# Kernel tuning notes

Hardware: AMD Instinct MI355X
Metric: run time of the kernel (lower is better)

## Reference

```python
import jax, jax.numpy as jnp
import numpy as np

N = 50000      # nodes
E = 600000     # edges (before self-loops)
F_IN = 128     # num_node_features
HID = 64       # hidden_channels
HEADS = 4      # num_heads
ACT = 32       # action_dim
SENT = 768     # sentence embedding dim (fc1 input)


def setup_inputs() -> dict:
    key = jax.random.key(0)
    ks = jax.random.split(key, 32)
    rn = lambda k, s, sc=0.05: jax.random.normal(k, s, jnp.float32) * sc
    return {
        "x": jax.random.normal(ks[0], (N, F_IN), jnp.float32),
        "edge_index": jax.random.randint(ks[1], (2, E), 0, N, dtype=jnp.int32),
        "sentence_emb": jax.random.normal(ks[2], (1, SENT), jnp.float32),
        "active_node_idx": 123,
        "step": 3,
        # conv1: GATConv(F_IN -> HID, heads=HEADS, concat=True)
        "W1": rn(ks[3], (F_IN, HEADS * HID)),
        "att_src1": rn(ks[4], (HEADS, HID)),
        "att_dst1": rn(ks[5], (HEADS, HID)),
        "b1": jnp.zeros((HEADS * HID,), jnp.float32),
        # conv2: GATConv(HEADS*HID -> HID, heads=1, concat=False)
        "W2": rn(ks[6], (HEADS * HID, HID)),
        "att_src2": rn(ks[7], (1, HID)),
        "att_dst2": rn(ks[8], (1, HID)),
        "b2": jnp.zeros((HID,), jnp.float32),
        "fc0_w": rn(ks[9], (1, HID)), "fc0_b": jnp.zeros((HID,), jnp.float32),
        "fc1_w": rn(ks[10], (SENT, HID)), "fc1_b": jnp.zeros((HID,), jnp.float32),
        "fc2_w": rn(ks[11], (HID, HID)), "fc2_b": jnp.zeros((HID,), jnp.float32),
        "fc3_w": rn(ks[12], (2 * HID, HID)), "fc3_b": jnp.zeros((HID,), jnp.float32),
        "val_w": rn(ks[13], (HID, 1)), "val_b": jnp.zeros((1,), jnp.float32),
        "adv_w": rn(ks[14], (HID, ACT)), "adv_b": jnp.zeros((ACT,), jnp.float32),
        "ln_h_g": jnp.ones((HID,), jnp.float32), "ln_h_b": jnp.zeros((HID,), jnp.float32),
        "ln_f_g": jnp.ones((2 * HID,), jnp.float32), "ln_f_b": jnp.zeros((2 * HID,), jnp.float32),
        "ln_a_g": jnp.ones((HEADS * HID,), jnp.float32), "ln_a_b": jnp.zeros((HEADS * HID,), jnp.float32),
    }


def layernorm(x, g, b, eps=1e-5):
    mu = jnp.mean(x, axis=-1, keepdims=True)
    var = jnp.mean((x - mu) ** 2, axis=-1, keepdims=True)
    return (x - mu) / jnp.sqrt(var + eps) * g + b


def gat_layer(h_in, src, dst, W, a_src, a_dst, bias, concat):
    """PyG GATConv (eval mode): gather -> edge score -> segment softmax -> scatter-add."""
    n = h_in.shape[0]
    heads, ch = a_src.shape
    h = (h_in @ W).reshape(n, heads, ch)                      # [N,H,C]
    es = jnp.einsum('nhc,hc->nh', h, a_src)                   # alpha_src per node
    ed = jnp.einsum('nhc,hc->nh', h, a_dst)                   # alpha_dst per node
    e = jax.nn.leaky_relu(es[src] + ed[dst], 0.2)             # [Etot,H]
    m = jax.ops.segment_max(e, dst, num_segments=n)           # stable softmax per dst
    ex = jnp.exp(e - m[dst])
    denom = jax.ops.segment_sum(ex, dst, num_segments=n) + 1e-16
    alpha = ex / denom[dst]                                   # [Etot,H]
    out = jax.ops.segment_sum(h[src] * alpha[:, :, None], dst, num_segments=n)
    out = out.reshape(n, heads * ch) if concat else out.mean(axis=1)
    return out + bias, alpha


def reference(x, edge_index, sentence_emb, active_node_idx, step,
              W1, att_src1, att_dst1, b1, W2, att_src2, att_dst2, b2,
              fc0_w, fc0_b, fc1_w, fc1_b, fc2_w, fc2_b, fc3_w, fc3_b,
              val_w, val_b, adv_w, adv_b,
              ln_h_g, ln_h_b, ln_f_g, ln_f_b, ln_a_g, ln_a_b):
    n = x.shape[0]
    loops = jnp.arange(n, dtype=edge_index.dtype)             # PyG add_self_loops=True
    src = jnp.concatenate([edge_index[0], loops])
    dst = jnp.concatenate([edge_index[1], loops])

    # step embedding: fc0((step+1)*0.01) -> relu -> LN
    steps = jnp.full((1, 1), (step + 1) * 0.01, jnp.float32)
    steps = layernorm(jax.nn.relu(steps @ fc0_w + fc0_b), ln_h_g, ln_h_b)

    # sentence embedding path (F.normalize result is discarded in the original)
    sent = layernorm(jax.nn.relu(sentence_emb @ fc1_w + fc1_b), ln_h_g, ln_h_b)
    sent = sent + steps
    sent = layernorm(jax.nn.relu(sent @ fc2_w + fc2_b), ln_h_g, ln_h_b)

    # two GAT layers
    h1, _ = gat_layer(x, src, dst, W1, att_src1, att_dst1, b1, concat=True)
    h1 = layernorm(jax.nn.elu(h1), ln_a_g, ln_a_b)
    h2, alpha = gat_layer(h1, src, dst, W2, att_src2, att_dst2, b2, concat=False)
    h2 = layernorm(h2, ln_h_g, ln_h_b)

    # dueling head on active node
    anf = jnp.concatenate([h2[active_node_idx][None, :], sent], axis=1)   # [1, 2*HID]
    anf = layernorm(anf, ln_f_g, ln_f_b)
    anf = layernorm(jax.nn.relu(anf @ fc3_w + fc3_b), ln_h_g, ln_h_b)
    val = anf @ val_w + val_b
    adv = anf @ adv_w + adv_b
    logits = jnp.tanh(val + adv - adv.mean())
    return logits, h2, alpha
```

## Files before the change

kernel.cpp:

```cpp
#include <hip/hip_runtime.h>
#include <cstdint>
#include <cstddef>

#define DEV __device__ __forceinline__

static constexpr int NN  = 50000;
static constexpr int EE  = 600000;
static constexpr int ET  = 650000;
static constexpr int CAP = 96;

typedef __attribute__((ext_vector_type(8))) short bf16x8;
typedef __attribute__((ext_vector_type(4))) float f32x4;
typedef __attribute__((ext_vector_type(4))) int   i32x4;

DEV float wsum(float v){
  #pragma unroll
  for (int o = 32; o > 0; o >>= 1) v += __shfl_xor(v, o, 64);
  return v;
}
DEV float wmaxr(float v){
  #pragma unroll
  for (int o = 32; o > 0; o >>= 1) v = fmaxf(v, __shfl_xor(v, o, 64));
  return v;
}
DEV float lrelu(float x){ return x > 0.f ? x : 0.2f * x; }
DEV float eluf(float x){ return x > 0.f ? x : expm1f(x); }
DEV float ln64(float v, const float* g, const float* b, int lane){
  float mu  = wsum(v) * (1.f/64.f);
  float d   = v - mu;
  float var = wsum(d*d) * (1.f/64.f);
  return d * rsqrtf(var + 1e-5f) * g[lane] + b[lane];
}
DEV unsigned int bf16u(float f){
  unsigned int u = __float_as_uint(f);
  return (u + 0x7fffu + ((u >> 16) & 1u)) >> 16;
}
DEV float bfl(unsigned int lo16){ return __uint_as_float(lo16 << 16); }

__global__ void bucket_fill(const int* __restrict__ ei,
                            int* __restrict__ cnt,
                            int* __restrict__ bucket){
  int e = blockIdx.x * blockDim.x + threadIdx.x;
  if (e >= ET) return;
  int src, dst;
  if (e < EE){ src = ei[e]; dst = ei[EE + e]; } else { src = dst = e - EE; }
  int pos = atomicAdd(&cnt[dst], 1);
  if (pos < CAP) bucket[(size_t)dst * CAP + pos] = src;
}

__global__ __launch_bounds__(256) void pack_both(const float* __restrict__ W1,
                                                 const float* __restrict__ W2,
                                                 short* __restrict__ Wp1,
                                                 short* __restrict__ Wp2){
  int tid = blockIdx.x * 256 + threadIdx.x;
  if (tid < 4096){
    int lane = tid & 63, ks = (tid >> 6) & 3, mb = tid >> 8;
    int col  = mb * 16 + (lane & 15);
    int krow = ks * 32 + (lane >> 4) * 8;
    #pragma unroll
    for (int j = 0; j < 8; j++)
      Wp1[(size_t)tid * 8 + j] = (short)bf16u(W1[(size_t)(krow + j) * 256 + col]);
  } else if (tid < 4096 + 2048){
    int t2 = tid - 4096;
    int lane = t2 & 63, ks = (t2 >> 6) & 7, mb = t2 >> 9;
    int col  = mb * 16 + (lane & 15);
    int krow = ks * 32 + (lane >> 4) * 8;
    #pragma unroll
    for (int j = 0; j < 8; j++)
      Wp2[(size_t)t2 * 8 + j] = (short)bf16u(W2[(size_t)(krow + j) * 64 + col]);
  }
}

template<int KSTEPS, int MBLKS, int NH, bool INF32>
__global__ __launch_bounds__(256) void mfma_gemm_att(const short* __restrict__ Wp,
                                                     const float* __restrict__ Xf,
                                                     const unsigned short* __restrict__ Xh,
                                                     unsigned short* __restrict__ Cb,
                                                     const float* __restrict__ asrc,
                                                     const float* __restrict__ adst,
                                                     float* __restrict__ es,
                                                     float* __restrict__ ed, int M){
  constexpr int K = KSTEPS * 32, N = MBLKS * 16;
  int lane  = threadIdx.x & 63;
  int wv    = threadIdx.x >> 6;
  int quad  = lane >> 4;
  int node  = blockIdx.x * 64 + wv * 16 + (lane & 15);
  bool nv   = node < M;
  int nodec = nv ? node : M - 1;

  f32x4 acc[MBLKS];
  #pragma unroll
  for (int m = 0; m < MBLKS; m++) acc[m] = (f32x4){0.f, 0.f, 0.f, 0.f};

  #pragma unroll
  for (int ks = 0; ks < KSTEPS; ks++){
    int k0 = ks * 32 + quad * 8;
    bf16x8 bfrag;
    if (INF32){
      float4 u = *(const float4*)(Xf + (size_t)nodec * K + k0);
      float4 v = *(const float4*)(Xf + (size_t)nodec * K + k0 + 4);
      i32x4 bi;
      bi.x = (int)(bf16u(u.x) | (bf16u(u.y) << 16));
      bi.y = (int)(bf16u(u.z) | (bf16u(u.w) << 16));
      bi.z = (int)(bf16u(v.x) | (bf16u(v.y) << 16));
      bi.w = (int)(bf16u(v.z) | (bf16u(v.w) << 16));
      bfrag = __builtin_bit_cast(bf16x8, bi);
    } else {
      bfrag = *(const bf16x8*)(Xh + (size_t)nodec * K + k0);
    }
    #pragma unroll
    for (int mb = 0; mb < MBLKS; mb++){
      bf16x8 afrag = *(const bf16x8*)(Wp + ((size_t)(mb * KSTEPS + ks) * 64 + lane) * 8);
      acc[mb] = __builtin_amdgcn_mfma_f32_16x16x32_bf16(afrag, bfrag, acc[mb], 0, 0, 0);
    }
  }

  if (nv){
    unsigned short* crow = Cb + (size_t)node * N;
    #pragma unroll
    for (int mb = 0; mb < MBLKS; mb++){
      uint2 p;
      p.x = bf16u(acc[mb][0]) | (bf16u(acc[mb][1]) << 16);
      p.y = bf16u(acc[mb][2]) | (bf16u(acc[mb][3]) << 16);
      *(uint2*)(crow + mb * 16 + quad * 4) = p;
    }
  }

  float ps[NH], pd[NH];
  #pragma unroll
  for (int h = 0; h < NH; h++){ ps[h] = 0.f; pd[h] = 0.f; }
  #pragma unroll
  for (int mb = 0; mb < MBLKS; mb++){
    int h = (NH == 1) ? 0 : (mb >> 2);
    #pragma unroll
    for (int r = 0; r < 4; r++){
      int c = mb * 16 + quad * 4 + r;
      ps[h] = fmaf(acc[mb][r], asrc[c], ps[h]);
      pd[h] = fmaf(acc[mb][r], adst[c], pd[h]);
    }
  }
  #pragma unroll
  for (int h = 0; h < NH; h++){
    ps[h] += __shfl_xor(ps[h], 16, 64); ps[h] += __shfl_xor(ps[h], 32, 64);
    pd[h] += __shfl_xor(pd[h], 16, 64); pd[h] += __shfl_xor(pd[h], 32, 64);
  }
  if (quad == 0 && nv){
    if (NH == 4){
      *(float4*)(es + (size_t)node * 4) = make_float4(ps[0], ps[1], ps[2], ps[3]);
      *(float4*)(ed + (size_t)node * 4) = make_float4(pd[0], pd[1], pd[2], pd[3]);
    } else {
      es[node] = ps[0];
      ed[node] = pd[0];
    }
  }
}

DEV void acc4u(uint2 g, float q, float& ax, float& ay, float& az, float& aw){
  ax = fmaf(__uint_as_float(g.x << 16),         q, ax);
  ay = fmaf(__uint_as_float(g.x & 0xffff0000u), q, ay);
  az = fmaf(__uint_as_float(g.y << 16),         q, az);
  aw = fmaf(__uint_as_float(g.y & 0xffff0000u), q, aw);
}

__global__ __launch_bounds__(256) void agg1_kernel(const int* __restrict__ cnt,
                                                   const int* __restrict__ bucket,
                                                   const unsigned short* __restrict__ H1b,
                                                   const float* __restrict__ es,
                                                   const float* __restrict__ ed,
                                                   const float* __restrict__ b1,
                                                   const float* __restrict__ lng,
                                                   const float* __restrict__ lnb,
                                                   unsigned short* __restrict__ h1b, int n){
  __shared__ float wsh4[4][64][4];
  __shared__ int   ssh[4][64];
  int wv   = threadIdx.x >> 6;
  int wid  = (blockIdx.x * blockDim.x + threadIdx.x) >> 6;
  int lane = threadIdx.x & 63;
  if (wid >= n) return;
  int deg = min(cnt[wid], CAP);
  const int* base = bucket + (size_t)wid * CAP;
  const float4 edv = *(const float4*)(ed + (size_t)wid * 4);

  float v0, v1, v2, v3;

  if (deg <= 64){
    bool vld = lane < deg;
    int srcl = vld ? base[lane] : 0;
    float4 e4 = vld ? *(const float4*)(es + (size_t)srcl * 4)
                    : make_float4(-1e30f, -1e30f, -1e30f, -1e30f);
    float e0 = vld ? lrelu(e4.x + edv.x) : -1e30f;
    float e1 = vld ? lrelu(e4.y + edv.y) : -1e30f;
    float e2 = vld ? lrelu(e4.z + edv.z) : -1e30f;
    float e3 = vld ? lrelu(e4.w + edv.w) : -1e30f;
    float m0 = wmaxr(e0), m1 = wmaxr(e1), m2 = wmaxr(e2), m3 = wmaxr(e3);
    float w0 = vld ? __expf(e0 - m0) : 0.f;
    float w1 = vld ? __expf(e1 - m1) : 0.f;
    float w2 = vld ? __expf(e2 - m2) : 0.f;
    float w3 = vld ? __expf(e3 - m3) : 0.f;
    w0 /= (wsum(w0) + 1e-16f);
    w1 /= (wsum(w1) + 1e-16f);
    w2 /= (wsum(w2) + 1e-16f);
    w3 /= (wsum(w3) + 1e-16f);
    ssh[wv][lane] = srcl;
    *(float4*)&wsh4[wv][lane][0] = make_float4(w0, w1, w2, w3);
    __builtin_amdgcn_wave_barrier();

    int h = lane >> 4;
    int lane4 = lane * 4;
    float ax = 0.f, ay = 0.f, az = 0.f, aw = 0.f;
    int t = 0;
    for (; t + 4 <= deg; t += 4){
      int a0 = ssh[wv][t],     a1 = ssh[wv][t + 1];
      int a2 = ssh[wv][t + 2], a3 = ssh[wv][t + 3];
      float q0 = wsh4[wv][t][h],     q1 = wsh4[wv][t + 1][h];
      float q2 = wsh4[wv][t + 2][h], q3 = wsh4[wv][t + 3][h];
      uint2 g0 = *(const uint2*)(H1b + (size_t)a0 * 256 + lane4);
      uint2 g1 = *(const uint2*)(H1b + (size_t)a1 * 256 + lane4);
      uint2 g2 = *(const uint2*)(H1b + (size_t)a2 * 256 + lane4);
      uint2 g3 = *(const uint2*)(H1b + (size_t)a3 * 256 + lane4);
      acc4u(g0, q0, ax, ay, az, aw);
      acc4u(g1, q1, ax, ay, az, aw);
      acc4u(g2, q2, ax, ay, az, aw);
      acc4u(g3, q3, ax, ay, az, aw);
    }
    for (; t < deg; t++){
      int a0 = ssh[wv][t];
      float q0 = wsh4[wv][t][h];
      uint2 g0 = *(const uint2*)(H1b + (size_t)a0 * 256 + lane4);
      acc4u(g0, q0, ax, ay, az, aw);
    }
    float4 bb = *(const float4*)(b1 + lane4);
    v0 = eluf(ax + bb.x); v1 = eluf(ay + bb.y);
    v2 = eluf(az + bb.z); v3 = eluf(aw + bb.w);
    float mu = wsum(v0 + v1 + v2 + v3) * (1.f/256.f);
    float q  = (v0-mu)*(v0-mu) + (v1-mu)*(v1-mu) + (v2-mu)*(v2-mu) + (v3-mu)*(v3-mu);
    float rstd = rsqrtf(wsum(q) * (1.f/256.f) + 1e-5f);
    float4 g4v = *(const float4*)(lng + lane4);
    float4 bo  = *(const float4*)(lnb + lane4);
    uint2 p;
    p.x = bf16u((v0-mu)*rstd*g4v.x + bo.x) | (bf16u((v1-mu)*rstd*g4v.y + bo.y) << 16);
    p.y = bf16u((v2-mu)*rstd*g4v.z + bo.z) | (bf16u((v3-mu)*rstd*g4v.w + bo.w) << 16);
    *(uint2*)(h1b + (size_t)wid * 256 + lane4) = p;
    return;
  }

  float m0 = -1e30f, m1 = -1e30f, m2 = -1e30f, m3 = -1e30f;
  for (int j = lane; j < deg; j += 64){
    int src = base[j];
    float4 e4 = *(const float4*)(es + (size_t)src * 4);
    m0 = fmaxf(m0, lrelu(e4.x + edv.x));
    m1 = fmaxf(m1, lrelu(e4.y + edv.y));
    m2 = fmaxf(m2, lrelu(e4.z + edv.z));
    m3 = fmaxf(m3, lrelu(e4.w + edv.w));
  }
  m0 = wmaxr(m0); m1 = wmaxr(m1); m2 = wmaxr(m2); m3 = wmaxr(m3);
  float acc0 = 0.f, acc1 = 0.f, acc2 = 0.f, acc3 = 0.f;
  float den0 = 0.f, den1 = 0.f, den2 = 0.f, den3 = 0.f;
  for (int j = 0; j < deg; j++){
    int src = base[j];
    float4 e4 = *(const float4*)(es + (size_t)src * 4);
    float x0 = __expf(lrelu(e4.x + edv.x) - m0);
    float x1 = __expf(lrelu(e4.y + edv.y) - m1);
    float x2 = __expf(lrelu(e4.z + edv.z) - m2);
    float x3 = __expf(lrelu(e4.w + edv.w) - m3);
    den0 += x0; den1 += x1; den2 += x2; den3 += x3;
    const unsigned short* hp = H1b + (size_t)src * 256;
    acc0 = fmaf(bfl(hp[lane]),       x0, acc0);
    acc1 = fmaf(bfl(hp[64 + lane]),  x1, acc1);
    acc2 = fmaf(bfl(hp[128 + lane]), x2, acc2);
    acc3 = fmaf(bfl(hp[192 + lane]), x3, acc3);
  }
  v0 = eluf(acc0 / (den0 + 1e-16f) + b1[lane]);
  v1 = eluf(acc1 / (den1 + 1e-16f) + b1[64 + lane]);
  v2 = eluf(acc2 / (den2 + 1e-16f) + b1[128 + lane]);
  v3 = eluf(acc3 / (den3 + 1e-16f) + b1[192 + lane]);
  float mu = wsum(v0 + v1 + v2 + v3) * (1.f/256.f);
  float q  = (v0-mu)*(v0-mu) + (v1-mu)*(v1-mu) + (v2-mu)*(v2-mu) + (v3-mu)*(v3-mu);
  float rstd = rsqrtf(wsum(q) * (1.f/256.f) + 1e-5f);
  unsigned short* o = h1b + (size_t)wid * 256;
  o[lane]       = (unsigned short)bf16u((v0-mu)*rstd*lng[lane]       + lnb[lane]);
  o[64 + lane]  = (unsigned short)bf16u((v1-mu)*rstd*lng[64 + lane]  + lnb[64 + lane]);
  o[128 + lane] = (unsigned short)bf16u((v2-mu)*rstd*lng[128 + lane] + lnb[128 + lane]);
  o[192 + lane] = (unsigned short)bf16u((v3-mu)*rstd*lng[192 + lane] + lnb[192 + lane]);
}

DEV float agg2_slow(const int* base, int deg, float edv,
                    const unsigned short* H2b, const float* es,
                    int lane, float& m_out, float& den_out){
  float m = -1e30f;
  for (int j = lane; j < deg; j += 64)
    m = fmaxf(m, lrelu(es[base[j]] + edv));
  m = wmaxr(m);
  float den = 0.f;
  for (int j = lane; j < deg; j += 64)
    den += __expf(lrelu(es[base[j]] + edv) - m);
  den = wsum(den) + 1e-16f;
  float acc = 0.f;
  for (int j = 0; j < deg; j++){
    int src = base[j];
    float a = __expf(lrelu(es[src] + edv) - m) / den;
    acc = fmaf(bfl(H2b[(size_t)src * 64 + lane]), a, acc);
  }
  m_out = m; den_out = den;
  return acc;
}

__global__ __launch_bounds__(256) void agg2_head(const int* __restrict__ cnt,
                                                 const int* __restrict__ bucket,
                                                 const unsigned short* __restrict__ H2b,
                                                 const float* __restrict__ es,
                                                 const float* __restrict__ ed,
                                                 const float* __restrict__ b2,
                                                 const float* __restrict__ lng,
                                                 const float* __restrict__ lnb,
                                                 const float* __restrict__ semb,
                                                 const int* __restrict__ active,
                                                 const int* __restrict__ stepp,
                                                 const float* __restrict__ fc0w, const float* __restrict__ fc0b,
                                                 const float* __restrict__ fc1w, const float* __restrict__ fc1b,
                                                 const float* __restrict__ fc2w, const float* __restrict__ fc2b,
                                                 const float* __restrict__ fc3w, const float* __restrict__ fc3b,
                                                 const float* __restrict__ valw, const float* __restrict__ valb,
                                                 const float* __restrict__ advw, const float* __restrict__ advb,
                                                 const float* __restrict__ lnhg, const float* __restrict__ lnhb,
                                                 const float* __restrict__ lnfg, const float* __restrict__ lnfb,
                                                 float* __restrict__ h2out,
                                                 float2* __restrict__ mden,
                                                 float* __restrict__ logits, int n){
  __shared__ float shh[192];
  int wpair = (blockIdx.x * blockDim.x + threadIdx.x) >> 6;
  int lane  = threadIdx.x & 63;
  int n0 = wpair * 2, n1 = wpair * 2 + 1;
  if (n0 >= n) return;
  bool has1 = n1 < n;

  int deg0 = min(cnt[n0], CAP);
  int deg1 = has1 ? min(cnt[n1], CAP) : 0;
  const int* base0 = bucket + (size_t)n0 * CAP;
  const int* base1 = bucket + (size_t)n1 * CAP;
  float edv0 = ed[n0];
  float edv1 = has1 ? ed[n1] : 0.f;
  float acc0 = 0.f, acc1 = 0.f;

  if (deg0 <= 64 && deg1 <= 64){
    bool v0 = lane < deg0;
    int s0 = v0 ? base0[lane] : 0;
    float e0 = v0 ? lrelu(es[s0] + edv0) : -1e30f;
    float m0 = wmaxr(e0);
    float w0 = v0 ? __expf(e0 - m0) : 0.f;
    float den0 = wsum(w0) + 1e-16f;
    float wl0 = v0 ? w0 / den0 : 0.f;
    bool v1 = lane < deg1;
    int s1 = v1 ? base1[lane] : 0;
    float e1 = v1 ? lrelu(es[s1] + edv1) : -1e30f;
    float m1 = wmaxr(e1);
    float w1 = v1 ? __expf(e1 - m1) : 0.f;
    float den1 = wsum(w1) + 1e-16f;
    float wl1 = v1 ? w1 / den1 : 0.f;
    if (lane == 0){
      mden[n0] = make_float2(m0, den0);
      if (has1) mden[n1] = make_float2(m1, den1);
    }

    int dmax = max(deg0, deg1);
    int t = 0;
    for (; t + 2 <= dmax; t += 2){
      int a00 = __shfl(s0, t, 64),   a01 = __shfl(s0, t + 1, 64);
      int a10 = __shfl(s1, t, 64),   a11 = __shfl(s1, t + 1, 64);
      float q00 = __shfl(wl0, t, 64), q01 = __shfl(wl0, t + 1, 64);
      float q10 = __shfl(wl1, t, 64), q11 = __shfl(wl1, t + 1, 64);
      float h00 = bfl(H2b[(size_t)a00 * 64 + lane]);
      float h01 = bfl(H2b[(size_t)a01 * 64 + lane]);
      float h10 = bfl(H2b[(size_t)a10 * 64 + lane]);
      float h11 = bfl(H2b[(size_t)a11 * 64 + lane]);
      acc0 = fmaf(h00, q00, acc0); acc0 = fmaf(h01, q01, acc0);
      acc1 = fmaf(h10, q10, acc1); acc1 = fmaf(h11, q11, acc1);
    }
    for (; t < dmax; t++){
      int a00 = __shfl(s0, t, 64);
      int a10 = __shfl(s1, t, 64);
      float q00 = __shfl(wl0, t, 64);
      float q10 = __shfl(wl1, t, 64);
      acc0 = fmaf(bfl(H2b[(size_t)a00 * 64 + lane]), q00, acc0);
      acc1 = fmaf(bfl(H2b[(size_t)a10 * 64 + lane]), q10, acc1);
    }
  } else {
    float m0, den0, m1 = 0.f, den1 = 1.f;
    acc0 = agg2_slow(base0, deg0, edv0, H2b, es, lane, m0, den0);
    if (has1) acc1 = agg2_slow(base1, deg1, edv1, H2b, es, lane, m1, den1);
    if (lane == 0){
      mden[n0] = make_float2(m0, den0);
      if (has1) mden[n1] = make_float2(m1, den1);
    }
  }

  float va = acc0 + b2[lane];
  float mua = wsum(va) * (1.f/64.f);
  float da = va - mua;
  float rsa = rsqrtf(wsum(da*da) * (1.f/64.f) + 1e-5f);
  float h2v0 = da * rsa * lng[lane] + lnb[lane];
  h2out[(size_t)n0 * 64 + lane] = h2v0;
  float h2v1 = 0.f;
  if (has1){
    float vb = acc1 + b2[lane];
    float mub = wsum(vb) * (1.f/64.f);
    float db = vb - mub;
    float rsb = rsqrtf(wsum(db*db) * (1.f/64.f) + 1e-5f);
    h2v1 = db * rsb * lng[lane] + lnb[lane];
    h2out[(size_t)n1 * 64 + lane] = h2v1;
  }

  int actv = active[0];
  if (n0 == actv || n1 == actv){
    int t = lane;
    float h2v = (n0 == actv) ? h2v0 : h2v1;

    float sval = (float)(stepp[0] + 1) * 0.01f;
    float stepsv = ln64(fmaxf(fmaf(sval, fc0w[t], fc0b[t]), 0.f), lnhg, lnhb, t);

    float acc1h = fc1b[t];
    #pragma unroll 8
    for (int k = 0; k < 768; k++) acc1h = fmaf(semb[k], fc1w[k * 64 + t], acc1h);
    float sentv = ln64(fmaxf(acc1h, 0.f), lnhg, lnhb, t) + stepsv;
    shh[t] = sentv;
    __builtin_amdgcn_wave_barrier();
    float acc2h = fc2b[t];
    #pragma unroll 8
    for (int k = 0; k < 64; k++) acc2h = fmaf(shh[k], fc2w[k * 64 + t], acc2h);
    __builtin_amdgcn_wave_barrier();
    float sent2 = ln64(fmaxf(acc2h, 0.f), lnhg, lnhb, t);

    float c0 = h2v, c1 = sent2;
    float mu2 = wsum(c0 + c1) * (1.f/128.f);
    float q2  = (c0-mu2)*(c0-mu2) + (c1-mu2)*(c1-mu2);
    float rs2 = rsqrtf(wsum(q2) * (1.f/128.f) + 1e-5f);
    shh[t]      = (c0-mu2)*rs2*lnfg[t]      + lnfb[t];
    shh[64 + t] = (c1-mu2)*rs2*lnfg[64 + t] + lnfb[64 + t];
    __builtin_amdgcn_wave_barrier();

    float acc3h = fc3b[t];
    #pragma unroll 8
    for (int k = 0; k < 128; k++) acc3h = fmaf(shh[k], fc3w[k * 64 + t], acc3h);
    float a2v = ln64(fmaxf(acc3h, 0.f), lnhg, lnhb, t);
    shh[128 + t] = a2v;
    __builtin_amdgcn_wave_barrier();

    float val = wsum(a2v * valw[t]) + valb[0];
    float advv = 0.f;
    if (t < 32){
      advv = advb[t];
      #pragma unroll 8
      for (int k = 0; k < 64; k++) advv = fmaf(shh[128 + k], advw[k * 32 + t], advv);
    }
    float am = wsum(t < 32 ? advv : 0.f) * (1.f/32.f);
    if (t < 32) logits[t] = tanhf(val + advv - am);
  }
}

__global__ __launch_bounds__(256) void edge_alpha(const int* __restrict__ ei,
                                                  const float* __restrict__ es,
                                                  const float* __restrict__ ed,
                                                  const float2* __restrict__ mden,
                                                  float* __restrict__ alpha_out){
  int e = blockIdx.x * blockDim.x + threadIdx.x;
  if (e >= ET) return;
  int src, dst;
  if (e < EE){ src = ei[e]; dst = ei[EE + e]; } else { src = dst = e - EE; }
  float2 md = mden[dst];
  float sc = lrelu(es[src] + ed[dst]);
  alpha_out[e] = __expf(sc - md.x) / md.y;
}

extern "C" void kernel_launch(void* const* d_in, const int* in_sizes, int n_in,
                              void* d_out, int out_size, void* d_ws, size_t ws_size,
                              hipStream_t stream) {
  const float* x     = (const float*)d_in[0];
  const int*   ei    = (const int*)  d_in[1];
  const float* semb  = (const float*)d_in[2];
  const int*   act   = (const int*)  d_in[3];
  const int*   step  = (const int*)  d_in[4];
  const float* W1    = (const float*)d_in[5];
  const float* as1   = (const float*)d_in[6];
  const float* ad1   = (const float*)d_in[7];
  const float* b1    = (const float*)d_in[8];
  const float* W2    = (const float*)d_in[9];
  const float* as2   = (const float*)d_in[10];
  const float* ad2   = (const float*)d_in[11];
  const float* b2    = (const float*)d_in[12];
  const float* fc0w  = (const float*)d_in[13];
  const float* fc0b  = (const float*)d_in[14];
  const float* fc1w  = (const float*)d_in[15];
  const float* fc1b  = (const float*)d_in[16];
  const float* fc2w  = (const float*)d_in[17];
  const float* fc2b  = (const float*)d_in[18];
  const float* fc3w  = (const float*)d_in[19];
  const float* fc3b  = (const float*)d_in[20];
  const float* valw  = (const float*)d_in[21];
  const float* valb  = (const float*)d_in[22];
  const float* advw  = (const float*)d_in[23];
  const float* advb  = (const float*)d_in[24];
  const float* lnhg  = (const float*)d_in[25];
  const float* lnhb  = (const float*)d_in[26];
  const float* lnfg  = (const float*)d_in[27];
  const float* lnfb  = (const float*)d_in[28];
  const float* lnag  = (const float*)d_in[29];
  const float* lnab  = (const float*)d_in[30];

  char* ws = (char*)d_ws;
  size_t o = 0;
  auto alloc = [&](size_t bytes) -> void* {
    o = (o + 255) & ~(size_t)255;
    void* p = ws + o;
    o += bytes;
    return p;
  };
  int*   cnt     = (int*)  alloc((size_t)NN * 4);
  int*   bucket  = (int*)  alloc((size_t)NN * CAP * 4);
  short* Wp1     = (short*)alloc((size_t)4096 * 8 * 2);
  short* Wp2     = (short*)alloc((size_t)2048 * 8 * 2);
  unsigned short* H1b = (unsigned short*)alloc((size_t)NN * 256 * 2);
  unsigned short* h1b = (unsigned short*)alloc((size_t)NN * 256 * 2);
  float* es1     = (float*)alloc((size_t)NN * 16);
  float* ed1     = (float*)alloc((size_t)NN * 16);
  float2* mden   = (float2*)alloc((size_t)NN * 8);
  unsigned short* H2b = H1b;
  float* es2 = es1;
  float* ed2 = ed1;

  float* logits    = (float*)d_out;
  float* h2out     = (float*)d_out + 32;
  float* alpha_out = (float*)d_out + 32 + (size_t)NN * 64;

  hipMemsetAsync(cnt, 0, (size_t)NN * 4, stream);
  bucket_fill<<<(ET + 255) / 256, 256, 0, stream>>>(ei, cnt, bucket);
  pack_both<<<24, 256, 0, stream>>>(W1, W2, Wp1, Wp2);

  mfma_gemm_att<4, 16, 4, true><<<(NN + 63) / 64, 256, 0, stream>>>(
      Wp1, x, nullptr, H1b, as1, ad1, es1, ed1, NN);
  agg1_kernel<<<NN / 4, 256, 0, stream>>>(cnt, bucket, H1b, es1, ed1, b1, lnag, lnab, h1b, NN);

  mfma_gemm_att<8, 4, 1, false><<<(NN + 63) / 64, 256, 0, stream>>>(
      Wp2, nullptr, h1b, H2b, as2, ad2, es2, ed2, NN);
  agg2_head<<<(NN + 7) / 8, 256, 0, stream>>>(cnt, bucket, H2b, es2, ed2, b2,
                                              lnhg, lnhb,
                                              semb, act, step,
                                              fc0w, fc0b, fc1w, fc1b, fc2w, fc2b, fc3w, fc3b,
                                              valw, valb, advw, advb,
                                              lnhg, lnhb, lnfg, lnfb,
                                              h2out, mden, logits, NN);
  edge_alpha<<<(ET + 255) / 256, 256, 0, stream>>>(ei, es2, ed2, mden, alpha_out);
}
```

Before: 336.4 us.

## Restructure layer-2 aggregation to one node per wave with paired-edge bf16x2 gathers

The second GAT aggregation kernel now gives each wavefront one destination node instead of two and doubles the grid to match. Edge indices and softmax weights are staged in LDS. Each half-wave handles alternate edges and loads two bf16 channels per lane as one 32-bit word, and the halves are combined with a cross-half shuffle. The aim is fewer, wider gather instructions and more independent loads in flight per wave, at the cost of more waves, LDS traffic and an extra reduction step.

```diff
diff --git a/kernel.cpp b/kernel.cpp
--- a/kernel.cpp
+++ b/kernel.cpp
@@ -328,92 +328,82 @@
                                                  float2* __restrict__ mden,
                                                  float* __restrict__ logits, int n){
   __shared__ float shh[192];
-  int wpair = (blockIdx.x * blockDim.x + threadIdx.x) >> 6;
-  int lane  = threadIdx.x & 63;
-  int n0 = wpair * 2, n1 = wpair * 2 + 1;
-  if (n0 >= n) return;
-  bool has1 = n1 < n;
-
-  int deg0 = min(cnt[n0], CAP);
-  int deg1 = has1 ? min(cnt[n1], CAP) : 0;
-  const int* base0 = bucket + (size_t)n0 * CAP;
-  const int* base1 = bucket + (size_t)n1 * CAP;
-  float edv0 = ed[n0];
-  float edv1 = has1 ? ed[n1] : 0.f;
-  float acc0 = 0.f, acc1 = 0.f;
-
-  if (deg0 <= 64 && deg1 <= 64){
-    bool v0 = lane < deg0;
-    int s0 = v0 ? base0[lane] : 0;
-    float e0 = v0 ? lrelu(es[s0] + edv0) : -1e30f;
+  __shared__ int   ssh[4][64];
+  __shared__ float wsh[4][64];
+  int wv   = threadIdx.x >> 6;
+  int node = (blockIdx.x * blockDim.x + threadIdx.x) >> 6;
+  int lane = threadIdx.x & 63;
+  if (node >= n) return;
+
+  int p  = lane >> 5;
+  int c0 = (lane & 31) * 2;
+
+  int deg = min(cnt[node], CAP);
+  const int* base = bucket + (size_t)node * CAP;
+  float edv = ed[node];
+
+  float2 a = make_float2(0.f, 0.f);
+
+  if (deg <= 64){
+    bool vld = lane < deg;
+    int s0 = vld ? base[lane] : 0;
+    float e0 = vld ? lrelu(es[s0] + edv) : -1e30f;
     float m0 = wmaxr(e0);
-    float w0 = v0 ? __expf(e0 - m0) : 0.f;
+    float w0 = vld ? __expf(e0 - m0) : 0.f;
     float den0 = wsum(w0) + 1e-16f;
-    float wl0 = v0 ? w0 / den0 : 0.f;
-    bool v1 = lane < deg1;
-    int s1 = v1 ? base1[lane] : 0;
-    float e1 = v1 ? lrelu(es[s1] + edv1) : -1e30f;
-    float m1 = wmaxr(e1);
-    float w1 = v1 ? __expf(e1 - m1) : 0.f;
-    float den1 = wsum(w1) + 1e-16f;
-    float wl1 = v1 ? w1 / den1 : 0.f;
-    if (lane == 0){
-      mden[n0] = make_float2(m0, den0);
-      if (has1) mden[n1] = make_float2(m1, den1);
-    }
-
-    int dmax = max(deg0, deg1);
-    int t = 0;
-    for (; t + 2 <= dmax; t += 2){
-      int a00 = __shfl(s0, t, 64),   a01 = __shfl(s0, t + 1, 64);
-      int a10 = __shfl(s1, t, 64),   a11 = __shfl(s1, t + 1, 64);
-      float q00 = __shfl(wl0, t, 64), q01 = __shfl(wl0, t + 1, 64);
-      float q10 = __shfl(wl1, t, 64), q11 = __shfl(wl1, t + 1, 64);
-      float h00 = bfl(H2b[(size_t)a00 * 64 + lane]);
-      float h01 = bfl(H2b[(size_t)a01 * 64 + lane]);
-      float h10 = bfl(H2b[(size_t)a10 * 64 + lane]);
-      float h11 = bfl(H2b[(size_t)a11 * 64 + lane]);
-      acc0 = fmaf(h00, q00, acc0); acc0 = fmaf(h01, q01, acc0);
-      acc1 = fmaf(h10, q10, acc1); acc1 = fmaf(h11, q11, acc1);
-    }
-    for (; t < dmax; t++){
-      int a00 = __shfl(s0, t, 64);
-      int a10 = __shfl(s1, t, 64);
-      float q00 = __shfl(wl0, t, 64);
-      float q10 = __shfl(wl1, t, 64);
-      acc0 = fmaf(bfl(H2b[(size_t)a00 * 64 + lane]), q00, acc0);
-      acc1 = fmaf(bfl(H2b[(size_t)a10 * 64 + lane]), q10, acc1);
-    }
+    float wl0 = w0 / den0;
+    if (lane == 0) mden[node] = make_float2(m0, den0);
+
+    ssh[wv][lane] = s0;
+    wsh[wv][lane] = wl0;
+    __builtin_amdgcn_wave_barrier();
+
+    int dpad = (deg + 7) & ~7;
+    for (int t = 0; t < dpad; t += 8){
+      int   i0 = ssh[wv][t     + p], i1 = ssh[wv][t + 2 + p];
+      int   i2 = ssh[wv][t + 4 + p], i3 = ssh[wv][t + 6 + p];
+      float q0 = wsh[wv][t     + p], q1 = wsh[wv][t + 2 + p];
+      float q2 = wsh[wv][t + 4 + p], q3 = wsh[wv][t + 6 + p];
+      unsigned int g0 = *(const unsigned int*)(H2b + (size_t)i0 * 64 + c0);
+      unsigned int g1 = *(const unsigned int*)(H2b + (size_t)i1 * 64 + c0);
+      unsigned int g2 = *(const unsigned int*)(H2b + (size_t)i2 * 64 + c0);
+      unsigned int g3 = *(const unsigned int*)(H2b + (size_t)i3 * 64 + c0);
+      a.x = fmaf(__uint_as_float(g0 << 16),         q0, a.x);
+      a.y = fmaf(__uint_as_float(g0 & 0xffff0000u), q0, a.y);
+      a.x = fmaf(__uint_as_float(g1 << 16),         q1, a.x);
+      a.y = fmaf(__uint_as_float(g1 & 0xffff0000u), q1, a.y);
+      a.x = fmaf(__uint_as_float(g2 << 16),         q2, a.x);
+      a.y = fmaf(__uint_as_float(g2 & 0xffff0000u), q2, a.y);
+      a.x = fmaf(__uint_as_float(g3 << 16),         q3, a.x);
+      a.y = fmaf(__uint_as_float(g3 & 0xffff0000u), q3, a.y);
+    }
+    a.x += __shfl_xor(a.x, 32, 64);
+    a.y += __shfl_xor(a.y, 32, 64);
   } else {
-    float m0, den0, m1 = 0.f, den1 = 1.f;
-    acc0 = agg2_slow(base0, deg0, edv0, H2b, es, lane, m0, den0);
-    if (has1) acc1 = agg2_slow(base1, deg1, edv1, H2b, es, lane, m1, den1);
-    if (lane == 0){
-      mden[n0] = make_float2(m0, den0);
-      if (has1) mden[n1] = make_float2(m1, den1);
-    }
-  }
-
-  float va = acc0 + b2[lane];
-  float mua = wsum(va) * (1.f/64.f);
-  float da = va - mua;
-  float rsa = rsqrtf(wsum(da*da) * (1.f/64.f) + 1e-5f);
-  float h2v0 = da * rsa * lng[lane] + lnb[lane];
-  h2out[(size_t)n0 * 64 + lane] = h2v0;
-  float h2v1 = 0.f;
-  if (has1){
-    float vb = acc1 + b2[lane];
-    float mub = wsum(vb) * (1.f/64.f);
-    float db = vb - mub;
-    float rsb = rsqrtf(wsum(db*db) * (1.f/64.f) + 1e-5f);
-    h2v1 = db * rsb * lng[lane] + lnb[lane];
-    h2out[(size_t)n1 * 64 + lane] = h2v1;
-  }
-
-  int actv = active[0];
-  if (n0 == actv || n1 == actv){
+    float m0, den0;
+    float accc = agg2_slow(base, deg, edv, H2b, es, lane, m0, den0);
+    if (lane == 0) mden[node] = make_float2(m0, den0);
+    a.x = __shfl(accc, c0, 64);
+    a.y = __shfl(accc, c0 + 1, 64);
+  }
+
+  float2 bb = *(const float2*)(b2 + c0);
+  float vx = a.x + bb.x, vy = a.y + bb.y;
+  float mu = wsum(vx + vy) * (1.f/128.f);
+  float dx = vx - mu, dy = vy - mu;
+  float rs = rsqrtf(wsum(dx*dx + dy*dy) * (1.f/128.f) + 1e-5f);
+  float2 gg = *(const float2*)(lng + c0);
+  float2 bo = *(const float2*)(lnb + c0);
+  float hx = dx * rs * gg.x + bo.x;
+  float hy = dy * rs * gg.y + bo.y;
+  if (p == 0) *(float2*)(h2out + (size_t)node * 64 + c0) = make_float2(hx, hy);
+
+  if (node == active[0]){
+    if (p == 0) *(float2*)&shh[128 + c0] = make_float2(hx, hy);
+    __builtin_amdgcn_wave_barrier();
     int t = lane;
-    float h2v = (n0 == actv) ? h2v0 : h2v1;
+    float h2v = shh[128 + t];
+    __builtin_amdgcn_wave_barrier();
 
     float sval = (float)(stepp[0] + 1) * 0.01f;
     float stepsv = ln64(fmaxf(fmaf(sval, fc0w[t], fc0b[t]), 0.f), lnhg, lnhb, t);
@@ -430,12 +420,12 @@
     __builtin_amdgcn_wave_barrier();
     float sent2 = ln64(fmaxf(acc2h, 0.f), lnhg, lnhb, t);
 
-    float c0 = h2v, c1 = sent2;
-    float mu2 = wsum(c0 + c1) * (1.f/128.f);
-    float q2  = (c0-mu2)*(c0-mu2) + (c1-mu2)*(c1-mu2);
+    float c0h = h2v, c1h = sent2;
+    float mu2 = wsum(c0h + c1h) * (1.f/128.f);
+    float q2  = (c0h-mu2)*(c0h-mu2) + (c1h-mu2)*(c1h-mu2);
     float rs2 = rsqrtf(wsum(q2) * (1.f/128.f) + 1e-5f);
-    shh[t]      = (c0-mu2)*rs2*lnfg[t]      + lnfb[t];
-    shh[64 + t] = (c1-mu2)*rs2*lnfg[64 + t] + lnfb[64 + t];
+    shh[t]      = (c0h-mu2)*rs2*lnfg[t]      + lnfb[t];
+    shh[64 + t] = (c1h-mu2)*rs2*lnfg[64 + t] + lnfb[64 + t];
     __builtin_amdgcn_wave_barrier();
 
     float acc3h = fc3b[t];
@@ -541,7 +531,7 @@
 
   mfma_gemm_att<8, 4, 1, false><<<(NN + 63) / 64, 256, 0, stream>>>(
       Wp2, nullptr, h1b, H2b, as2, ad2, es2, ed2, NN);
-  agg2_head<<<(NN + 7) / 8, 256, 0, stream>>>(cnt, bucket, H2b, es2, ed2, b2,
+  agg2_head<<<(NN + 3) / 4, 256, 0, stream>>>(cnt, bucket, H2b, es2, ed2, b2,
                                               lnhg, lnhb,
                                               semb, act, step,
                                               fc0w, fc0b, fc1w, fc1b, fc2w, fc2b, fc3w, fc3b,
```

After: 336.4 us. Within noise of the previous version (+0.0%).
